# Optimization experiments

Measured on AMD Instinct MI355X. Metric: run time of the kernel, lower is better.

Reference implementation:

```python
import jax, jax.numpy as jnp
import numpy as np

EPS = 1e-5
NUM_GRAPHS = 64


def _linear(x, W, b):
    return x @ W + b


def setup_inputs() -> dict:
    key = jax.random.key(0)
    ks = jax.random.split(key, 32)
    N, E, IN, EF, H, ED, T, L, C = 25000, 400000, 128, 16, 32, 32, 4, 2, 1
    F = H            # F_in (divide_input=False)
    Fo = H // T      # F_out per tower

    def w(k, shape):
        return jax.random.normal(k, shape, jnp.float32) / np.sqrt(shape[-2])

    inp = {
        'x': jax.random.normal(ks[0], (N, IN), jnp.float32),
        'edge_attr': jax.random.normal(ks[1], (E, EF), jnp.float32),
        'edge_weight': jax.random.uniform(ks[2], (E,), jnp.float32),
        'edge_index': jax.random.randint(ks[3], (2, E), 0, N),
        'batch': jnp.sort(jax.random.randint(ks[4], (N,), 0, NUM_GRAPHS)),
        'node_W': w(ks[5], (IN, H)), 'node_b': jnp.zeros((H,), jnp.float32),
        'edge_W': w(ks[6], (EF, ED)), 'edge_b': jnp.zeros((ED,), jnp.float32),
        'enc_W': w(ks[7], (L, ED, F)), 'enc_b': jnp.zeros((L, F), jnp.float32),
        'pre_W': w(ks[8], (L, T, 3 * F, F)), 'pre_b': jnp.zeros((L, T, F), jnp.float32),
        'post_W': w(ks[9], (L, T, 13 * F, Fo)), 'post_b': jnp.zeros((L, T, Fo), jnp.float32),
        'lin_W': w(ks[10], (L, H, H)), 'lin_b': jnp.zeros((L, H), jnp.float32),
        'bn_g': jnp.ones((L, H), jnp.float32), 'bn_b': jnp.zeros((L, H), jnp.float32),
        'mlp_W1': w(ks[11], (H, H)), 'mlp_b1': jnp.zeros((H,), jnp.float32),
        'mlp_W2': w(ks[12], (H, H // 2)), 'mlp_b2': jnp.zeros((H // 2,), jnp.float32),
        'mlp_W3': w(ks[13], (H // 2, C)), 'mlp_b3': jnp.zeros((C,), jnp.float32),
    }
    return inp


def reference(x, edge_attr, edge_weight, node_W, node_b, edge_W, edge_b,
              enc_W, enc_b, pre_W, pre_b, post_W, post_b, lin_W, lin_b,
              bn_g, bn_b, mlp_W1, mlp_b1, mlp_W2, mlp_b2, mlp_W3, mlp_b3,
              edge_index, batch):
    N = x.shape[0]
    L, T = pre_W.shape[0], pre_W.shape[1]
    src, dst = edge_index[0], edge_index[1]

    # degree-based scalers (PNA): avg_deg_log = mean_n log(deg_n + 1)
    deg = jax.ops.segment_sum(jnp.ones((src.shape[0],), x.dtype), dst, num_segments=N)
    avg_deg_log = jnp.mean(jnp.log(deg + 1.0))
    degc = jnp.clip(deg, 1.0)[:, None, None]          # [N,1,1]
    log_deg = jnp.log(degc + 1.0)
    amp = log_deg / avg_deg_log                        # amplification scaler
    att = avg_deg_log / log_deg                        # attenuation scaler
    has_edge = (deg > 0)[:, None, None]

    h = _linear(x, node_W, node_b)                     # node_emb  [N,H]
    e = _linear(edge_attr, edge_W, edge_b)             # edge_emb  [E,ED]

    for l in range(L):
        el = _linear(e, enc_W[l], enc_b[l])            # edge_encoder [E,F]
        m_in = jnp.concatenate([h[dst], h[src], el], axis=-1)      # [E,3F]
        msg = jnp.einsum('ef,tfg->etg', m_in, pre_W[l]) + pre_b[l]  # per-tower pre_nn [E,T,F]
        msg = msg * edge_weight[:, None, None]
        s = jax.ops.segment_sum(msg, dst, num_segments=N)
        s2 = jax.ops.segment_sum(msg * msg, dst, num_segments=N)
        mean = s / degc
        std = jnp.sqrt(jax.nn.relu(s2 / degc - mean * mean) + EPS)
        mn = jnp.where(has_edge, jax.ops.segment_min(msg, dst, num_segments=N), 0.0)
        mx = jnp.where(has_edge, jax.ops.segment_max(msg, dst, num_segments=N), 0.0)
        agg = jnp.concatenate([mean, mn, mx, std], axis=-1)            # [N,T,4F]
        agg = jnp.concatenate([agg, agg * amp, agg * att], axis=-1)    # [N,T,12F]
        out = jnp.concatenate(
            [jnp.broadcast_to(h[:, None, :], (N, T, h.shape[-1])), agg], axis=-1)  # [N,T,13F]
        out = jnp.einsum('ntf,tfg->ntg', out, post_W[l]) + post_b[l]   # post_nn [N,T,Fo]
        out = out.reshape(N, -1) @ lin_W[l] + lin_b[l]                 # [N,H]
        mu = jnp.mean(out, axis=0)
        var = jnp.var(out, axis=0)
        out = (out - mu) / jnp.sqrt(var + EPS) * bn_g[l] + bn_b[l]     # BatchNorm (batch stats)
        h = jax.nn.relu(out)

    g = jax.ops.segment_sum(h, batch, num_segments=NUM_GRAPHS)        # global_add_pool
    g = jax.nn.relu(_linear(g, mlp_W1, mlp_b1))
    g = jax.nn.relu(_linear(g, mlp_W2, mlp_b2))
    return _linear(g, mlp_W3, mlp_b3)
```

## Files before the change

kernel.cpp:

```cpp
#include <hip/hip_runtime.h>

constexpr float kEps = 1e-5f;

__device__ __forceinline__ unsigned short f2bf(float x) {
  unsigned int u = __float_as_uint(x);
  unsigned int r = (u + 0x7fffu + ((u >> 16) & 1u)) >> 16;
  return (unsigned short)r;
}
__device__ __forceinline__ float bflo(unsigned int u) { return __uint_as_float(u << 16); }
__device__ __forceinline__ float bfhi(unsigned int u) { return __uint_as_float(u & 0xffff0000u); }
__device__ __forceinline__ unsigned int packbf(float a, float b) {
  return (unsigned int)f2bf(a) | ((unsigned int)f2bf(b) << 16);
}


__global__ void zero_int2(int* __restrict__ a, int* __restrict__ b, int n) {
  int i = blockIdx.x * blockDim.x + threadIdx.x;
  if (i < n) { a[i] = 0; b[i] = 0; }
}

__global__ void hist_kernel(const int* __restrict__ dst, int* __restrict__ deg, int E) {
  int e = blockIdx.x * blockDim.x + threadIdx.x;
  if (e < E) atomicAdd(&deg[dst[e]], 1);
}

__global__ void scan1_kernel(const int* __restrict__ deg, int* __restrict__ off,
                             int* __restrict__ part, int N) {
  __shared__ int sm[1024];
  int i = blockIdx.x * 1024 + threadIdx.x;
  int v = (i < N) ? deg[i] : 0;
  sm[threadIdx.x] = v;
  __syncthreads();
  for (int o = 1; o < 1024; o <<= 1) {
    int t = (threadIdx.x >= o) ? sm[threadIdx.x - o] : 0;
    __syncthreads();
    sm[threadIdx.x] += t;
    __syncthreads();
  }
  if (i < N) off[i] = sm[threadIdx.x] - v;
  if (threadIdx.x == 1023) part[blockIdx.x] = sm[1023];
}

__global__ void scan2_kernel(int* __restrict__ part, int* __restrict__ off, int nb, int N) {
  if (threadIdx.x == 0) {
    int run = 0;
    for (int b = 0; b < nb; b++) { int p = part[b]; part[b] = run; run += p; }
    off[N] = run;
  }
}

__global__ void scan3_kernel(int* __restrict__ off, const int* __restrict__ part, int N) {
  int i = blockIdx.x * 1024 + threadIdx.x;
  if (i < N) off[i] += part[blockIdx.x];
}

__global__ void fill_kernel(const int* __restrict__ src, const int* __restrict__ dst,
                            const float* __restrict__ ew, const int* __restrict__ off,
                            int* __restrict__ cnt, int* __restrict__ edg,
                            int* __restrict__ srcs, float* __restrict__ ews, int E) {
  int e = blockIdx.x * blockDim.x + threadIdx.x;
  if (e < E) {
    int d = dst[e];
    int slot = off[d] + atomicAdd(&cnt[d], 1);
    edg[slot] = e;
    srcs[slot] = src[e];
    ews[slot] = ew[e];
  }
}

__global__ void egather_kernel(const int* __restrict__ edg, const float4* __restrict__ eattr4,
                               float4* __restrict__ eattrg4, int E4) {
  int i = blockIdx.x * blockDim.x + threadIdx.x;
  if (i < E4) {
    int slot = i >> 2, quad = i & 3;
    int e = edg[slot];
    eattrg4[i] = eattr4[e * 4 + quad];
  }
}

__global__ void adl_kernel(const int* __restrict__ deg, float* __restrict__ adl, int N) {
  __shared__ float sm[1024];
  float s = 0.f;
  for (int n = threadIdx.x; n < N; n += 1024) s += logf((float)deg[n] + 1.f);
  sm[threadIdx.x] = s;
  __syncthreads();
  for (int o = 512; o > 0; o >>= 1) {
    if (threadIdx.x < o) sm[threadIdx.x] += sm[threadIdx.x + o];
    __syncthreads();
  }
  if (threadIdx.x == 0) adl[0] = sm[0];
}

__global__ void node_emb_kernel(const float* __restrict__ x, const float* __restrict__ W,
                                const float* __restrict__ b, float* __restrict__ h, int N) {
  int n = blockIdx.x * 8 + (threadIdx.x >> 5);
  int j = threadIdx.x & 31;
  if (n >= N) return;
  float acc = b[j];
  const float4* x4 = (const float4*)(x + (size_t)n * 128);
#pragma unroll
  for (int q = 0; q < 32; q++) {
    float4 v = x4[q];
    acc += v.x * W[(4 * q + 0) * 32 + j];
    acc += v.y * W[(4 * q + 1) * 32 + j];
    acc += v.z * W[(4 * q + 2) * 32 + j];
    acc += v.w * W[(4 * q + 3) * 32 + j];
  }
  h[n * 32 + j] = acc;
}

__global__ void fuse_kernel(const float* __restrict__ edge_W, const float* __restrict__ edge_b,
                            const float* __restrict__ enc_W, const float* __restrict__ enc_b,
                            const float* __restrict__ pre_W, const float* __restrict__ pre_b,
                            float* __restrict__ Wf, float* __restrict__ bf) {
  __shared__ float tW[2][16][32];
  __shared__ float tb[2][32];
  int tid = threadIdx.x;
  for (int i = tid; i < 1024; i += 256) {
    int l = i >> 9, r = (i >> 5) & 15, c = i & 31;
    float s = 0.f;
    for (int k = 0; k < 32; k++) s += edge_W[r * 32 + k] * enc_W[(l * 32 + k) * 32 + c];
    tW[l][r][c] = s;
  }
  for (int i = tid; i < 64; i += 256) {
    int l = i >> 5, c = i & 31;
    float s = enc_b[l * 32 + c];
    for (int k = 0; k < 32; k++) s += edge_b[k] * enc_W[(l * 32 + k) * 32 + c];
    tb[l][c] = s;
  }
  __syncthreads();
  for (int i = tid; i < 4096; i += 256) {
    int l = i >> 11, t = (i >> 9) & 3, r = (i >> 5) & 15, c = i & 31;
    float s = 0.f;
    for (int k = 0; k < 32; k++) s += tW[l][r][k] * pre_W[((l * 4 + t) * 96 + 64 + k) * 32 + c];
    Wf[i] = s;
  }
  for (int i = tid; i < 256; i += 256) {
    int l = i >> 7, t = (i >> 5) & 3, c = i & 31;
    float s = pre_b[(l * 4 + t) * 32 + c];
    for (int k = 0; k < 32; k++) s += tb[l][k] * pre_W[((l * 4 + t) * 96 + 64 + k) * 32 + c];
    bf[i] = s;
  }
}

__global__ __launch_bounds__(256) void prep_kernel(
    const float* __restrict__ h, const float* __restrict__ preW,
    const float* __restrict__ bfv, unsigned short* __restrict__ qB,
    unsigned short* __restrict__ AB, float* __restrict__ bn, int N) {
  if (blockIdx.x == 0 && threadIdx.x < 64) bn[threadIdx.x] = 0.f;
  __shared__ float hs[16][32];
  int tid = threadIdx.x;
  int c = tid & 127, half = tid >> 7;
  int t = c >> 5, g = c & 31;
  float ws[32], wd[32];
  {
    const float* pS = preW + (t * 96 + 32) * 32 + g;
    const float* pD = preW + (t * 96) * 32 + g;
#pragma unroll
    for (int k = 0; k < 32; k++) { ws[k] = pS[k * 32]; wd[k] = pD[k * 32]; }
  }
  float bc = bfv[c];
  int base = blockIdx.x * 16;
  for (int i = tid; i < 512; i += 256) {
    int nn = i >> 5;
    hs[nn][i & 31] = (base + nn < N) ? h[(size_t)(base + nn) * 32 + (i & 31)] : 0.f;
  }
  __syncthreads();
#pragma unroll
  for (int nn = 0; nn < 8; ++nn) {
    int nl = half + 2 * nn;
    int n = base + nl;
    if (n >= N) continue;
    float qa = 0.f, Aa = bc;
#pragma unroll
    for (int k = 0; k < 32; k++) {
      float hk = hs[nl][k];
      qa = fmaf(hk, ws[k], qa);
      Aa = fmaf(hk, wd[k], Aa);
    }
    qB[(size_t)n * 128 + c] = f2bf(qa);
    AB[(size_t)n * 128 + c] = f2bf(Aa);
  }
}

#define FOLD8(F0, F1, VA, VB, O)                                           \
  F0 = fmaf(VA.x, wfa[O + 0], F0); F1 = fmaf(VA.x, wfb[O + 0], F1);        \
  F0 = fmaf(VA.y, wfa[O + 1], F0); F1 = fmaf(VA.y, wfb[O + 1], F1);        \
  F0 = fmaf(VA.z, wfa[O + 2], F0); F1 = fmaf(VA.z, wfb[O + 2], F1);        \
  F0 = fmaf(VA.w, wfa[O + 3], F0); F1 = fmaf(VA.w, wfb[O + 3], F1);        \
  F0 = fmaf(VB.x, wfa[O + 4], F0); F1 = fmaf(VB.x, wfb[O + 4], F1);        \
  F0 = fmaf(VB.y, wfa[O + 5], F0); F1 = fmaf(VB.y, wfb[O + 5], F1);        \
  F0 = fmaf(VB.z, wfa[O + 6], F0); F1 = fmaf(VB.z, wfb[O + 6], F1);        \
  F0 = fmaf(VB.w, wfa[O + 7], F0); F1 = fmaf(VB.w, wfb[O + 7], F1);

#define STATACC(V0, V1)                                                    \
  s0a += V0; sq0 = fmaf(V0, V0, sq0); mn0 = fminf(mn0, V0); mx0 = fmaxf(mx0, V0); \
  s1a += V1; sq1 = fmaf(V1, V1, sq1); mn1 = fminf(mn1, V1); mx1 = fmaxf(mx1, V1);

__global__ __launch_bounds__(256, 4) void agg3_kernel(
    const unsigned int* __restrict__ qB, const unsigned int* __restrict__ AB,
    const int* __restrict__ coff, const int* __restrict__ srcs,
    const float* __restrict__ ews, const float* __restrict__ eattrg,
    const float* __restrict__ Wf, unsigned int* __restrict__ stats, int N) {
  int lane = threadIdx.x & 63;
  int n = (blockIdx.x * blockDim.x + threadIdx.x) >> 6;
  if (n >= N) return;
  int t = lane >> 4, g0 = (2 * lane) & 31;
  float wfa[16], wfb[16];
  {
    const float* p = Wf + t * 512 + g0;
#pragma unroll
    for (int k = 0; k < 16; k++) { wfa[k] = p[k * 32]; wfb[k] = p[k * 32 + 1]; }
  }
  unsigned int au = AB[(size_t)n * 64 + lane];
  float a0 = bflo(au), a1 = bfhi(au);
  int beg = coff[n], end = coff[n + 1];
  int dg = end - beg;
  float s0a = 0.f, s1a = 0.f, sq0 = 0.f, sq1 = 0.f;
  float mn0 = 1e30f, mn1 = 1e30f, mx0 = -1e30f, mx1 = -1e30f;

  int i = beg;
  int sc0 = 0, sc1 = 0, sc2 = 0, sc3 = 0;
  if (i + 4 <= end) { sc0 = srcs[i]; sc1 = srcs[i + 1]; sc2 = srcs[i + 2]; sc3 = srcs[i + 3]; }
  for (; i + 4 <= end; i += 4) {
    unsigned int q0 = qB[(size_t)sc0 * 64 + lane];
    unsigned int q1 = qB[(size_t)sc1 * 64 + lane];
    unsigned int q2 = qB[(size_t)sc2 * 64 + lane];
    unsigned int q3 = qB[(size_t)sc3 * 64 + lane];
    float w0 = ews[i], w1 = ews[i + 1], w2 = ews[i + 2], w3 = ews[i + 3];
    const float4* ep = (const float4*)(eattrg + (size_t)i * 16);
    if (i + 8 <= end) { sc0 = srcs[i + 4]; sc1 = srcs[i + 5]; sc2 = srcs[i + 6]; sc3 = srcs[i + 7]; }
    float f00 = 0.f, f10 = 0.f, f01 = 0.f, f11 = 0.f;
    float f02 = 0.f, f12 = 0.f, f03 = 0.f, f13 = 0.f;
    {
      float4 aA = ep[0], aB = ep[1], bA = ep[4], bB = ep[5];
      float4 cA = ep[8], cB = ep[9], dA = ep[12], dB = ep[13];
      FOLD8(f00, f10, aA, aB, 0)
      FOLD8(f01, f11, bA, bB, 0)
      FOLD8(f02, f12, cA, cB, 0)
      FOLD8(f03, f13, dA, dB, 0)
    }
    {
      float4 aA = ep[2], aB = ep[3], bA = ep[6], bB = ep[7];
      float4 cA = ep[10], cB = ep[11], dA = ep[14], dB = ep[15];
      FOLD8(f00, f10, aA, aB, 8)
      FOLD8(f01, f11, bA, bB, 8)
      FOLD8(f02, f12, cA, cB, 8)
      FOLD8(f03, f13, dA, dB, 8)
    }
    float v0, v1;
    v0 = (a0 + bflo(q0) + f00) * w0; v1 = (a1 + bfhi(q0) + f10) * w0; STATACC(v0, v1)
    v0 = (a0 + bflo(q1) + f01) * w1; v1 = (a1 + bfhi(q1) + f11) * w1; STATACC(v0, v1)
    v0 = (a0 + bflo(q2) + f02) * w2; v1 = (a1 + bfhi(q2) + f12) * w2; STATACC(v0, v1)
    v0 = (a0 + bflo(q3) + f03) * w3; v1 = (a1 + bfhi(q3) + f13) * w3; STATACC(v0, v1)
  }
  for (; i < end; ++i) {
    int s = srcs[i];
    unsigned int q = qB[(size_t)s * 64 + lane];
    float w = ews[i];
    const float4* ep = (const float4*)(eattrg + (size_t)i * 16);
    float4 aA = ep[0], aB = ep[1], cA = ep[2], cB = ep[3];
    float f0 = 0.f, f1 = 0.f;
    FOLD8(f0, f1, aA, aB, 0)
    FOLD8(f0, f1, cA, cB, 8)
    float v0 = (a0 + bflo(q) + f0) * w;
    float v1 = (a1 + bfhi(q) + f1) * w;
    STATACC(v0, v1)
  }
  if (dg == 0) { mn0 = 0.f; mx0 = 0.f; mn1 = 0.f; mx1 = 0.f; }
  float inv = 1.f / (float)(dg > 0 ? dg : 1);
  float mean0 = s0a * inv, mean1 = s1a * inv;
  float sd0 = sqrtf(fmaxf(sq0 * inv - mean0 * mean0, 0.f) + kEps);
  float sd1 = sqrtf(fmaxf(sq1 * inv - mean1 * mean1, 0.f) + kEps);
  unsigned int* sp = stats + (size_t)n * 256;
  sp[0 * 64 + lane] = packbf(mean0, mean1);
  sp[1 * 64 + lane] = packbf(mn0, mn1);
  sp[2 * 64 + lane] = packbf(mx0, mx1);
  sp[3 * 64 + lane] = packbf(sd0, sd1);
}

__global__ __launch_bounds__(256) void post_kernel(
    const float* __restrict__ h, const unsigned int* __restrict__ stats,
    const int* __restrict__ coff, const float* __restrict__ adl,
    const float* __restrict__ postW, const float* __restrict__ postB,
    const float* __restrict__ linW, const float* __restrict__ linB,
    float* __restrict__ pre, float* __restrict__ bn, int N) {
  __shared__ unsigned int pwp[208 * 32];
  __shared__ unsigned int stu[4][256];
  __shared__ float red[8][32];
  int tid = threadIdx.x;
  for (int i = tid; i < 6656; i += 256) {
    int r = i >> 5, cc = i & 31, tP = cc >> 3, gq = cc & 7;
    float lo = postW[tP * 3328 + (2 * r) * 8 + gq];
    float hi = postW[tP * 3328 + (2 * r + 1) * 8 + gq];
    pwp[i] = packbf(lo, hi);
  }
  __syncthreads();

  int wave = tid >> 6, lane = tid & 63;
  int c = lane & 31, hh = lane >> 5;
  int tP = c >> 3;
  float adN = adl[0];
  float bs = 0.f, bq = 0.f;

  for (int n = blockIdx.x * 4 + wave; n < N; n += gridDim.x * 4) {
    {
      uint4 su = ((const uint4*)stats)[(size_t)n * 64 + lane];
      ((uint4*)stu[wave])[lane] = su;
    }
    int dg = coff[n + 1] - coff[n];
    float degc = (float)(dg > 0 ? dg : 1);
    float ad = adN / (float)N;
    float ld = logf(degc + 1.f);
    float amp = ld / ad, att = ad / ld;

    float acc = (hh == 0) ? postB[tP * 8 + (c & 7)] : 0.f;
    const float4* h4 = (const float4*)(h + (size_t)n * 32);
#pragma unroll
    for (int q4 = 0; q4 < 4; q4++) {
      float4 hv = h4[hh * 4 + q4];
      int r0 = hh * 8 + q4 * 2;
      unsigned int u0 = pwp[r0 * 32 + c], u1 = pwp[(r0 + 1) * 32 + c];
      acc = fmaf(hv.x, bflo(u0), acc);
      acc = fmaf(hv.y, bfhi(u0), acc);
      acc = fmaf(hv.z, bflo(u1), acc);
      acc = fmaf(hv.w, bfhi(u1), acc);
    }
#pragma unroll 8
    for (int jj = 0; jj < 32; jj++) {
      int sIdx = hh * 2 + (jj >> 4);
      unsigned int sv = stu[wave][sIdx * 64 + tP * 16 + (jj & 15)];
      float v0 = bflo(sv), v1 = bfhi(sv);
      int rm = 16 + hh * 32 + jj, ra = 80 + hh * 32 + jj, rt = 144 + hh * 32 + jj;
      unsigned int um = pwp[rm * 32 + c];
      unsigned int ua = pwp[ra * 32 + c];
      unsigned int ut = pwp[rt * 32 + c];
      float w0 = bflo(um); w0 = fmaf(amp, bflo(ua), w0); w0 = fmaf(att, bflo(ut), w0);
      float w1 = bfhi(um); w1 = fmaf(amp, bfhi(ua), w1); w1 = fmaf(att, bfhi(ut), w1);
      acc = fmaf(v0, w0, acc);
      acc = fmaf(v1, w1, acc);
    }
    acc += __shfl_xor(acc, 32);
    float o = linB[c];
#pragma unroll
    for (int k = 0; k < 32; k++) {
      float a = __shfl(acc, k);
      o = fmaf(a, linW[k * 32 + c], o);
    }
    if (lane < 32) {
      pre[(size_t)n * 32 + c] = o;
      bs += o;
      bq = fmaf(o, o, bq);
    }
  }

  __syncthreads();
  if (lane < 32) {
    red[wave * 2 + 0][c] = bs;
    red[wave * 2 + 1][c] = bq;
  }
  __syncthreads();
  if (tid < 64) {
    int which = tid >> 5, cc = tid & 31;
    float s = red[0 * 2 + which][cc] + red[1 * 2 + which][cc] +
              red[2 * 2 + which][cc] + red[3 * 2 + which][cc];
    atomicAdd(&bn[which * 32 + cc], s);
  }
}

__global__ void bn_apply_kernel(const float* __restrict__ pre, const float* __restrict__ bn,
                                const float* __restrict__ gamma, const float* __restrict__ beta,
                                float* __restrict__ h, int N) {
  int i = blockIdx.x * 256 + threadIdx.x;
  if (i >= N * 32) return;
  int j = i & 31;
  float invN = 1.f / (float)N;
  float mu = bn[j] * invN;
  float var = bn[32 + j] * invN - mu * mu;
  float is = rsqrtf(var + kEps);
  float v = (pre[i] - mu) * is * gamma[j] + beta[j];
  h[i] = fmaxf(v, 0.f);
}


__device__ __forceinline__ int lower_bound_dev(const int* a, int n, int key) {
  int lo = 0, hi = n;
  while (lo < hi) {
    int m = (lo + hi) >> 1;
    if (a[m] < key) lo = m + 1; else hi = m;
  }
  return lo;
}

__global__ void pool_kernel(const float* __restrict__ h, const int* __restrict__ batch,
                            float* __restrict__ gp, int N) {
  int gi = blockIdx.x;
  int lo = lower_bound_dev(batch, N, gi);
  int hi = lower_bound_dev(batch, N, gi + 1);
  __shared__ float part[8][32];
  int j = threadIdx.x & 31, ch = threadIdx.x >> 5;
  float s = 0.f;
  for (int n = lo + ch; n < hi; n += 8) s += h[(size_t)n * 32 + j];
  part[ch][j] = s;
  __syncthreads();
  if (threadIdx.x < 32) {
    float t = 0.f;
    for (int c2 = 0; c2 < 8; c2++) t += part[c2][j];
    gp[gi * 32 + j] = t;
  }
}

__global__ void mlp_kernel(const float* __restrict__ gp,
                           const float* __restrict__ W1, const float* __restrict__ b1,
                           const float* __restrict__ W2, const float* __restrict__ b2,
                           const float* __restrict__ W3, const float* __restrict__ b3,
                           float* __restrict__ out) {
  __shared__ float g1[64 * 32];
  __shared__ float g2[64 * 16];
  int tid = threadIdx.x;
  for (int i = tid; i < 2048; i += 256) {
    int r = i >> 5, c = i & 31;
    float s = b1[c];
    for (int k = 0; k < 32; k++) s += gp[r * 32 + k] * W1[k * 32 + c];
    g1[i] = fmaxf(s, 0.f);
  }
  __syncthreads();
  for (int i = tid; i < 1024; i += 256) {
    int r = i >> 4, c = i & 15;
    float s = b2[c];
    for (int k = 0; k < 32; k++) s += g1[r * 32 + k] * W2[k * 16 + c];
    g2[i] = fmaxf(s, 0.f);
  }
  __syncthreads();
  if (tid < 64) {
    float s = b3[0];
    for (int k = 0; k < 16; k++) s += g2[tid * 16 + k] * W3[k];
    out[tid] = s;
  }
}


extern "C" void kernel_launch(void* const* d_in, const int* in_sizes, int n_in,
                              void* d_out, int out_size, void* d_ws, size_t ws_size,
                              hipStream_t stream) {
  (void)n_in; (void)out_size; (void)ws_size;
  const float* x     = (const float*)d_in[0];
  const float* eattr = (const float*)d_in[1];
  const float* ew    = (const float*)d_in[2];
  const int*   eidx  = (const int*)d_in[3];
  const int*   batch = (const int*)d_in[4];
  const float* nodeW = (const float*)d_in[5];
  const float* nodeB = (const float*)d_in[6];
  const float* edgeW = (const float*)d_in[7];
  const float* edgeB = (const float*)d_in[8];
  const float* encW  = (const float*)d_in[9];
  const float* encB  = (const float*)d_in[10];
  const float* preW  = (const float*)d_in[11];
  const float* preB  = (const float*)d_in[12];
  const float* postW = (const float*)d_in[13];
  const float* postB = (const float*)d_in[14];
  const float* linW  = (const float*)d_in[15];
  const float* linB  = (const float*)d_in[16];
  const float* bnG   = (const float*)d_in[17];
  const float* bnB   = (const float*)d_in[18];
  const float* W1    = (const float*)d_in[19];
  const float* b1    = (const float*)d_in[20];
  const float* W2    = (const float*)d_in[21];
  const float* b2    = (const float*)d_in[22];
  const float* W3    = (const float*)d_in[23];
  const float* b3    = (const float*)d_in[24];
  float* out = (float*)d_out;

  int N = in_sizes[0] / 128;
  int E = in_sizes[2];
  const int* srcp = eidx;
  const int* dstp = eidx + E;

  char* wsb = (char*)d_ws;
  size_t woff = 0;
  auto alloc = [&](size_t bytes) -> void* {
    void* p = (void*)(wsb + woff);
    woff += (bytes + 255) & ~(size_t)255;
    return p;
  };
  int* deg   = (int*)alloc((size_t)N * 4);
  int* cnt   = (int*)alloc((size_t)N * 4);
  int* coff  = (int*)alloc((size_t)(N + 1) * 4);
  int* part  = (int*)alloc(64 * 4);
  int* edg   = (int*)alloc((size_t)E * 4);
  int* srcs  = (int*)alloc((size_t)E * 4);
  float* ews = (float*)alloc((size_t)E * 4);
  float* eattrg = (float*)alloc((size_t)E * 16 * 4);
  float* h    = (float*)alloc((size_t)N * 32 * 4);
  float* pre  = (float*)alloc((size_t)N * 32 * 4);
  float* adl  = (float*)alloc(256);
  float* bn   = (float*)alloc(64 * 4);
  float* gp   = (float*)alloc(64 * 32 * 4);
  float* WfB  = (float*)alloc(2 * 4 * 16 * 32 * 4);
  float* bfB  = (float*)alloc(2 * 4 * 32 * 4);
  unsigned short* qB  = (unsigned short*)alloc((size_t)N * 128 * 2);
  unsigned short* AB  = (unsigned short*)alloc((size_t)N * 128 * 2);
  unsigned int* stats = (unsigned int*)alloc((size_t)N * 256 * 4);

  int nb = (N + 1023) / 1024;
  zero_int2<<<(N + 255) / 256, 256, 0, stream>>>(deg, cnt, N);
  hist_kernel<<<(E + 255) / 256, 256, 0, stream>>>(dstp, deg, E);
  scan1_kernel<<<nb, 1024, 0, stream>>>(deg, coff, part, N);
  scan2_kernel<<<1, 64, 0, stream>>>(part, coff, nb, N);
  scan3_kernel<<<nb, 1024, 0, stream>>>(coff, part, N);
  fill_kernel<<<(E + 255) / 256, 256, 0, stream>>>(srcp, dstp, ew, coff, cnt, edg, srcs, ews, E);
  egather_kernel<<<(E * 4 + 255) / 256, 256, 0, stream>>>(edg, (const float4*)eattr,
                                                          (float4*)eattrg, E * 4);
  adl_kernel<<<1, 1024, 0, stream>>>(deg, adl, N);
  node_emb_kernel<<<(N + 7) / 8, 256, 0, stream>>>(x, nodeW, nodeB, h, N);
  fuse_kernel<<<1, 256, 0, stream>>>(edgeW, edgeB, encW, encB, preW, preB, WfB, bfB);

  for (int l = 0; l < 2; l++) {
    prep_kernel<<<(N + 15) / 16, 256, 0, stream>>>(
        h, preW + (size_t)l * 12288, bfB + (size_t)l * 128, qB, AB, bn, N);
    agg3_kernel<<<(N + 3) / 4, 256, 0, stream>>>(
        (const unsigned int*)qB, (const unsigned int*)AB, coff, srcs, ews,
        eattrg, WfB + (size_t)l * 2048, stats, N);
    post_kernel<<<1280, 256, 0, stream>>>(
        h, stats, coff, adl,
        postW + (size_t)l * 13312, postB + (size_t)l * 32,
        linW + (size_t)l * 1024, linB + (size_t)l * 32, pre, bn, N);
    bn_apply_kernel<<<(N * 32 + 255) / 256, 256, 0, stream>>>(pre, bn, bnG + (size_t)l * 32,
                                                              bnB + (size_t)l * 32, h, N);
  }
  pool_kernel<<<64, 256, 0, stream>>>(h, batch, gp, N);
  mlp_kernel<<<1, 256, 0, stream>>>(gp, W1, b1, W2, b2, W3, b3, out);
}
```

Baseline: 453.4 us.

## Fuse edge-attr gather into fill, fuse BN apply with next prep, pack agg math

The edge-attribute gather now happens inside the CSR fill kernel, which removes the edg index array and one launch. The layer-0 batch-norm apply is fused into the layer-1 prep kernel, and the BN stat buffers are zeroed up front instead of inside prep. The aggregation kernel uses packed 2-wide float vector FMA/min/max, prefetches edge weights alongside sources, adds a sched barrier, and drops the occupancy hint from 4 to 3 blocks. The trade-off is fewer launches and less global memory traffic, at the cost of scattered 64-byte writes in fill and possibly lower agg occupancy.

```diff
diff --git a/kernel.cpp b/kernel.cpp
--- a/kernel.cpp
+++ b/kernel.cpp
@@ -1,6 +1,8 @@
 #include <hip/hip_runtime.h>
 
 constexpr float kEps = 1e-5f;
+
+typedef float f2v __attribute__((ext_vector_type(2)));
 
 __device__ __forceinline__ unsigned short f2bf(float x) {
   unsigned int u = __float_as_uint(x);
@@ -12,11 +14,18 @@
 __device__ __forceinline__ unsigned int packbf(float a, float b) {
   return (unsigned int)f2bf(a) | ((unsigned int)f2bf(b) << 16);
 }
-
-
-__global__ void zero_int2(int* __restrict__ a, int* __restrict__ b, int n) {
+__device__ __forceinline__ f2v fma2(f2v a, f2v b, f2v c) { return __builtin_elementwise_fma(a, b, c); }
+__device__ __forceinline__ f2v splat2(float x) { f2v r; r.x = x; r.y = x; return r; }
+__device__ __forceinline__ f2v unpk(unsigned int u) { f2v r; r.x = bflo(u); r.y = bfhi(u); return r; }
+__device__ __forceinline__ f2v min2(f2v a, f2v b) { return __builtin_elementwise_min(a, b); }
+__device__ __forceinline__ f2v max2(f2v a, f2v b) { return __builtin_elementwise_max(a, b); }
+
+
+__global__ void zero_kernel(int* __restrict__ a, int* __restrict__ b,
+                            float* __restrict__ bnb, int n) {
   int i = blockIdx.x * blockDim.x + threadIdx.x;
   if (i < n) { a[i] = 0; b[i] = 0; }
+  if (i < 128) bnb[i] = 0.f;
 }
 
 __global__ void hist_kernel(const int* __restrict__ dst, int* __restrict__ deg, int E) {
@@ -55,26 +64,22 @@
 }
 
 __global__ void fill_kernel(const int* __restrict__ src, const int* __restrict__ dst,
-                            const float* __restrict__ ew, const int* __restrict__ off,
-                            int* __restrict__ cnt, int* __restrict__ edg,
-                            int* __restrict__ srcs, float* __restrict__ ews, int E) {
+                            const float* __restrict__ ew, const float4* __restrict__ eattr4,
+                            const int* __restrict__ off, int* __restrict__ cnt,
+                            int* __restrict__ srcs, float* __restrict__ ews,
+                            float4* __restrict__ eattrg4, int E) {
   int e = blockIdx.x * blockDim.x + threadIdx.x;
   if (e < E) {
     int d = dst[e];
     int slot = off[d] + atomicAdd(&cnt[d], 1);
-    edg[slot] = e;
     srcs[slot] = src[e];
     ews[slot] = ew[e];
-  }
-}
-
-__global__ void egather_kernel(const int* __restrict__ edg, const float4* __restrict__ eattr4,
-                               float4* __restrict__ eattrg4, int E4) {
-  int i = blockIdx.x * blockDim.x + threadIdx.x;
-  if (i < E4) {
-    int slot = i >> 2, quad = i & 3;
-    int e = edg[slot];
-    eattrg4[i] = eattr4[e * 4 + quad];
+    float4 a = eattr4[e * 4 + 0], b = eattr4[e * 4 + 1];
+    float4 c = eattr4[e * 4 + 2], q = eattr4[e * 4 + 3];
+    eattrg4[(size_t)slot * 4 + 0] = a;
+    eattrg4[(size_t)slot * 4 + 1] = b;
+    eattrg4[(size_t)slot * 4 + 2] = c;
+    eattrg4[(size_t)slot * 4 + 3] = q;
   }
 }
 
@@ -146,8 +151,7 @@
 __global__ __launch_bounds__(256) void prep_kernel(
     const float* __restrict__ h, const float* __restrict__ preW,
     const float* __restrict__ bfv, unsigned short* __restrict__ qB,
-    unsigned short* __restrict__ AB, float* __restrict__ bn, int N) {
-  if (blockIdx.x == 0 && threadIdx.x < 64) bn[threadIdx.x] = 0.f;
+    unsigned short* __restrict__ AB, int N) {
   __shared__ float hs[16][32];
   int tid = threadIdx.x;
   int c = tid & 127, half = tid >> 7;
@@ -183,21 +187,71 @@
   }
 }
 
-#define FOLD8(F0, F1, VA, VB, O)                                           \
-  F0 = fmaf(VA.x, wfa[O + 0], F0); F1 = fmaf(VA.x, wfb[O + 0], F1);        \
-  F0 = fmaf(VA.y, wfa[O + 1], F0); F1 = fmaf(VA.y, wfb[O + 1], F1);        \
-  F0 = fmaf(VA.z, wfa[O + 2], F0); F1 = fmaf(VA.z, wfb[O + 2], F1);        \
-  F0 = fmaf(VA.w, wfa[O + 3], F0); F1 = fmaf(VA.w, wfb[O + 3], F1);        \
-  F0 = fmaf(VB.x, wfa[O + 4], F0); F1 = fmaf(VB.x, wfb[O + 4], F1);        \
-  F0 = fmaf(VB.y, wfa[O + 5], F0); F1 = fmaf(VB.y, wfb[O + 5], F1);        \
-  F0 = fmaf(VB.z, wfa[O + 6], F0); F1 = fmaf(VB.z, wfb[O + 6], F1);        \
-  F0 = fmaf(VB.w, wfa[O + 7], F0); F1 = fmaf(VB.w, wfb[O + 7], F1);
-
-#define STATACC(V0, V1)                                                    \
-  s0a += V0; sq0 = fmaf(V0, V0, sq0); mn0 = fminf(mn0, V0); mx0 = fmaxf(mx0, V0); \
-  s1a += V1; sq1 = fmaf(V1, V1, sq1); mn1 = fminf(mn1, V1); mx1 = fmaxf(mx1, V1);
-
-__global__ __launch_bounds__(256, 4) void agg3_kernel(
+__global__ __launch_bounds__(256) void bnprep_kernel(
+    const float* __restrict__ pre, const float* __restrict__ bnv,
+    const float* __restrict__ gamma, const float* __restrict__ beta,
+    const float* __restrict__ preW, const float* __restrict__ bfv,
+    float* __restrict__ h, unsigned short* __restrict__ qB,
+    unsigned short* __restrict__ AB, int N) {
+  __shared__ float hs[16][32];
+  int tid = threadIdx.x;
+  int base = blockIdx.x * 16;
+  float invN = 1.f / (float)N;
+  for (int idx = tid; idx < 512; idx += 256) {
+    int nn = idx >> 5, j = idx & 31;
+    int n = base + nn;
+    float v = 0.f;
+    if (n < N) {
+      float mu = bnv[j] * invN;
+      float var = bnv[32 + j] * invN - mu * mu;
+      float is = rsqrtf(var + kEps);
+      v = fmaxf((pre[(size_t)n * 32 + j] - mu) * is * gamma[j] + beta[j], 0.f);
+      h[(size_t)n * 32 + j] = v;
+    }
+    hs[nn][j] = v;
+  }
+  int c = tid & 127, half = tid >> 7;
+  int t = c >> 5, g = c & 31;
+  float ws[32], wd[32];
+  {
+    const float* pS = preW + (t * 96 + 32) * 32 + g;
+    const float* pD = preW + (t * 96) * 32 + g;
+#pragma unroll
+    for (int k = 0; k < 32; k++) { ws[k] = pS[k * 32]; wd[k] = pD[k * 32]; }
+  }
+  float bc = bfv[c];
+  __syncthreads();
+#pragma unroll
+  for (int nn = 0; nn < 8; ++nn) {
+    int nl = half + 2 * nn;
+    int n = base + nl;
+    if (n >= N) continue;
+    float qa = 0.f, Aa = bc;
+#pragma unroll
+    for (int k = 0; k < 32; k++) {
+      float hk = hs[nl][k];
+      qa = fmaf(hk, ws[k], qa);
+      Aa = fmaf(hk, wd[k], Aa);
+    }
+    qB[(size_t)n * 128 + c] = f2bf(qa);
+    AB[(size_t)n * 128 + c] = f2bf(Aa);
+  }
+}
+
+#define FOLDE(F, EA, EB, EC, ED)                                \
+  F = fma2(splat2(EA.x), wf[0], F);  F = fma2(splat2(EA.y), wf[1], F);  \
+  F = fma2(splat2(EA.z), wf[2], F);  F = fma2(splat2(EA.w), wf[3], F);  \
+  F = fma2(splat2(EB.x), wf[4], F);  F = fma2(splat2(EB.y), wf[5], F);  \
+  F = fma2(splat2(EB.z), wf[6], F);  F = fma2(splat2(EB.w), wf[7], F);  \
+  F = fma2(splat2(EC.x), wf[8], F);  F = fma2(splat2(EC.y), wf[9], F);  \
+  F = fma2(splat2(EC.z), wf[10], F); F = fma2(splat2(EC.w), wf[11], F); \
+  F = fma2(splat2(ED.x), wf[12], F); F = fma2(splat2(ED.y), wf[13], F); \
+  F = fma2(splat2(ED.z), wf[14], F); F = fma2(splat2(ED.w), wf[15], F);
+
+#define STAT2(V)                                                \
+  sum = sum + V; sq = fma2(V, V, sq); mn = min2(mn, V); mx = max2(mx, V);
+
+__global__ __launch_bounds__(256, 3) void agg4_kernel(
     const unsigned int* __restrict__ qB, const unsigned int* __restrict__ AB,
     const int* __restrict__ coff, const int* __restrict__ srcs,
     const float* __restrict__ ews, const float* __restrict__ eattrg,
@@ -206,76 +260,73 @@
   int n = (blockIdx.x * blockDim.x + threadIdx.x) >> 6;
   if (n >= N) return;
   int t = lane >> 4, g0 = (2 * lane) & 31;
-  float wfa[16], wfb[16];
+  f2v wf[16];
   {
     const float* p = Wf + t * 512 + g0;
 #pragma unroll
-    for (int k = 0; k < 16; k++) { wfa[k] = p[k * 32]; wfb[k] = p[k * 32 + 1]; }
-  }
-  unsigned int au = AB[(size_t)n * 64 + lane];
-  float a0 = bflo(au), a1 = bfhi(au);
+    for (int k = 0; k < 16; k++) { f2v r; r.x = p[k * 32]; r.y = p[k * 32 + 1]; wf[k] = r; }
+  }
+  f2v a = unpk(AB[(size_t)n * 64 + lane]);
   int beg = coff[n], end = coff[n + 1];
   int dg = end - beg;
-  float s0a = 0.f, s1a = 0.f, sq0 = 0.f, sq1 = 0.f;
-  float mn0 = 1e30f, mn1 = 1e30f, mx0 = -1e30f, mx1 = -1e30f;
+  f2v sum = splat2(0.f), sq = splat2(0.f);
+  f2v mn = splat2(1e30f), mx = splat2(-1e30f);
 
   int i = beg;
   int sc0 = 0, sc1 = 0, sc2 = 0, sc3 = 0;
-  if (i + 4 <= end) { sc0 = srcs[i]; sc1 = srcs[i + 1]; sc2 = srcs[i + 2]; sc3 = srcs[i + 3]; }
+  float w0 = 0.f, w1 = 0.f, w2 = 0.f, w3 = 0.f;
+  if (i + 4 <= end) {
+    sc0 = srcs[i]; sc1 = srcs[i + 1]; sc2 = srcs[i + 2]; sc3 = srcs[i + 3];
+    w0 = ews[i]; w1 = ews[i + 1]; w2 = ews[i + 2]; w3 = ews[i + 3];
+  }
   for (; i + 4 <= end; i += 4) {
     unsigned int q0 = qB[(size_t)sc0 * 64 + lane];
     unsigned int q1 = qB[(size_t)sc1 * 64 + lane];
     unsigned int q2 = qB[(size_t)sc2 * 64 + lane];
     unsigned int q3 = qB[(size_t)sc3 * 64 + lane];
-    float w0 = ews[i], w1 = ews[i + 1], w2 = ews[i + 2], w3 = ews[i + 3];
     const float4* ep = (const float4*)(eattrg + (size_t)i * 16);
-    if (i + 8 <= end) { sc0 = srcs[i + 4]; sc1 = srcs[i + 5]; sc2 = srcs[i + 6]; sc3 = srcs[i + 7]; }
-    float f00 = 0.f, f10 = 0.f, f01 = 0.f, f11 = 0.f;
-    float f02 = 0.f, f12 = 0.f, f03 = 0.f, f13 = 0.f;
-    {
-      float4 aA = ep[0], aB = ep[1], bA = ep[4], bB = ep[5];
-      float4 cA = ep[8], cB = ep[9], dA = ep[12], dB = ep[13];
-      FOLD8(f00, f10, aA, aB, 0)
-      FOLD8(f01, f11, bA, bB, 0)
-      FOLD8(f02, f12, cA, cB, 0)
-      FOLD8(f03, f13, dA, dB, 0)
-    }
-    {
-      float4 aA = ep[2], aB = ep[3], bA = ep[6], bB = ep[7];
-      float4 cA = ep[10], cB = ep[11], dA = ep[14], dB = ep[15];
-      FOLD8(f00, f10, aA, aB, 8)
-      FOLD8(f01, f11, bA, bB, 8)
-      FOLD8(f02, f12, cA, cB, 8)
-      FOLD8(f03, f13, dA, dB, 8)
-    }
-    float v0, v1;
-    v0 = (a0 + bflo(q0) + f00) * w0; v1 = (a1 + bfhi(q0) + f10) * w0; STATACC(v0, v1)
-    v0 = (a0 + bflo(q1) + f01) * w1; v1 = (a1 + bfhi(q1) + f11) * w1; STATACC(v0, v1)
-    v0 = (a0 + bflo(q2) + f02) * w2; v1 = (a1 + bfhi(q2) + f12) * w2; STATACC(v0, v1)
-    v0 = (a0 + bflo(q3) + f03) * w3; v1 = (a1 + bfhi(q3) + f13) * w3; STATACC(v0, v1)
+    float4 e0 = ep[0], e1 = ep[1], e2 = ep[2], e3 = ep[3];
+    float4 e4 = ep[4], e5 = ep[5], e6 = ep[6], e7 = ep[7];
+    float4 e8 = ep[8], e9 = ep[9], e10 = ep[10], e11 = ep[11];
+    float4 e12 = ep[12], e13 = ep[13], e14 = ep[14], e15 = ep[15];
+    float wc0 = w0, wc1 = w1, wc2 = w2, wc3 = w3;
+    if (i + 8 <= end) {
+      sc0 = srcs[i + 4]; sc1 = srcs[i + 5]; sc2 = srcs[i + 6]; sc3 = srcs[i + 7];
+      w0 = ews[i + 4]; w1 = ews[i + 5]; w2 = ews[i + 6]; w3 = ews[i + 7];
+    }
+    __builtin_amdgcn_sched_barrier(0);
+    f2v f0 = splat2(0.f), f1 = splat2(0.f), f2_ = splat2(0.f), f3 = splat2(0.f);
+    FOLDE(f0, e0, e1, e2, e3)
+    FOLDE(f1, e4, e5, e6, e7)
+    FOLDE(f2_, e8, e9, e10, e11)
+    FOLDE(f3, e12, e13, e14, e15)
+    f2v v;
+    v = (a + unpk(q0) + f0) * splat2(wc0); STAT2(v)
+    v = (a + unpk(q1) + f1) * splat2(wc1); STAT2(v)
+    v = (a + unpk(q2) + f2_) * splat2(wc2); STAT2(v)
+    v = (a + unpk(q3) + f3) * splat2(wc3); STAT2(v)
   }
   for (; i < end; ++i) {
     int s = srcs[i];
+    float w = ews[i];
     unsigned int q = qB[(size_t)s * 64 + lane];
-    float w = ews[i];
     const float4* ep = (const float4*)(eattrg + (size_t)i * 16);
-    float4 aA = ep[0], aB = ep[1], cA = ep[2], cB = ep[3];
-    float f0 = 0.f, f1 = 0.f;
-    FOLD8(f0, f1, aA, aB, 0)
-    FOLD8(f0, f1, cA, cB, 8)
-    float v0 = (a0 + bflo(q) + f0) * w;
-    float v1 = (a1 + bfhi(q) + f1) * w;
-    STATACC(v0, v1)
-  }
-  if (dg == 0) { mn0 = 0.f; mx0 = 0.f; mn1 = 0.f; mx1 = 0.f; }
+    float4 ea = ep[0], eb = ep[1], ec = ep[2], ed = ep[3];
+    f2v f = splat2(0.f);
+    FOLDE(f, ea, eb, ec, ed)
+    f2v v = (a + unpk(q) + f) * splat2(w);
+    STAT2(v)
+  }
+  if (dg == 0) { mn = splat2(0.f); mx = splat2(0.f); }
   float inv = 1.f / (float)(dg > 0 ? dg : 1);
-  float mean0 = s0a * inv, mean1 = s1a * inv;
-  float sd0 = sqrtf(fmaxf(sq0 * inv - mean0 * mean0, 0.f) + kEps);
-  float sd1 = sqrtf(fmaxf(sq1 * inv - mean1 * mean1, 0.f) + kEps);
+  f2v mean = sum * splat2(inv);
+  f2v var = sq * splat2(inv) - mean * mean;
+  float sd0 = sqrtf(fmaxf(var.x, 0.f) + kEps);
+  float sd1 = sqrtf(fmaxf(var.y, 0.f) + kEps);
   unsigned int* sp = stats + (size_t)n * 256;
-  sp[0 * 64 + lane] = packbf(mean0, mean1);
-  sp[1 * 64 + lane] = packbf(mn0, mn1);
-  sp[2 * 64 + lane] = packbf(mx0, mx1);
+  sp[0 * 64 + lane] = packbf(mean.x, mean.y);
+  sp[1 * 64 + lane] = packbf(mn.x, mn.y);
+  sp[2 * 64 + lane] = packbf(mx.x, mx.y);
   sp[3 * 64 + lane] = packbf(sd0, sd1);
 }
 
@@ -487,14 +538,13 @@
   int* cnt   = (int*)alloc((size_t)N * 4);
   int* coff  = (int*)alloc((size_t)(N + 1) * 4);
   int* part  = (int*)alloc(64 * 4);
-  int* edg   = (int*)alloc((size_t)E * 4);
   int* srcs  = (int*)alloc((size_t)E * 4);
   float* ews = (float*)alloc((size_t)E * 4);
   float* eattrg = (float*)alloc((size_t)E * 16 * 4);
   float* h    = (float*)alloc((size_t)N * 32 * 4);
   float* pre  = (float*)alloc((size_t)N * 32 * 4);
   float* adl  = (float*)alloc(256);
-  float* bn   = (float*)alloc(64 * 4);
+  float* bnbuf = (float*)alloc(2 * 64 * 4);
   float* gp   = (float*)alloc(64 * 32 * 4);
   float* WfB  = (float*)alloc(2 * 4 * 16 * 32 * 4);
   float* bfB  = (float*)alloc(2 * 4 * 32 * 4);
@@ -503,31 +553,34 @@
   unsigned int* stats = (unsigned int*)alloc((size_t)N * 256 * 4);
 
   int nb = (N + 1023) / 1024;
-  zero_int2<<<(N + 255) / 256, 256, 0, stream>>>(deg, cnt, N);
+  zero_kernel<<<(N + 255) / 256, 256, 0, stream>>>(deg, cnt, bnbuf, N);
   hist_kernel<<<(E + 255) / 256, 256, 0, stream>>>(dstp, deg, E);
   scan1_kernel<<<nb, 1024, 0, stream>>>(deg, coff, part, N);
   scan2_kernel<<<1, 64, 0, stream>>>(part, coff, nb, N);
   scan3_kernel<<<nb, 1024, 0, stream>>>(coff, part, N);
-  fill_kernel<<<(E + 255) / 256, 256, 0, stream>>>(srcp, dstp, ew, coff, cnt, edg, srcs, ews, E);
-  egather_kernel<<<(E * 4 + 255) / 256, 256, 0, stream>>>(edg, (const float4*)eattr,
-                                                          (float4*)eattrg, E * 4);
+  fill_kernel<<<(E + 255) / 256, 256, 0, stream>>>(srcp, dstp, ew, (const float4*)eattr,
+                                                   coff, cnt, srcs, ews, (float4*)eattrg, E);
   adl_kernel<<<1, 1024, 0, stream>>>(deg, adl, N);
   node_emb_kernel<<<(N + 7) / 8, 256, 0, stream>>>(x, nodeW, nodeB, h, N);
   fuse_kernel<<<1, 256, 0, stream>>>(edgeW, edgeB, encW, encB, preW, preB, WfB, bfB);
 
-  for (int l = 0; l < 2; l++) {
-    prep_kernel<<<(N + 15) / 16, 256, 0, stream>>>(
-        h, preW + (size_t)l * 12288, bfB + (size_t)l * 128, qB, AB, bn, N);
-    agg3_kernel<<<(N + 3) / 4, 256, 0, stream>>>(
-        (const unsigned int*)qB, (const unsigned int*)AB, coff, srcs, ews,
-        eattrg, WfB + (size_t)l * 2048, stats, N);
-    post_kernel<<<1280, 256, 0, stream>>>(
-        h, stats, coff, adl,
-        postW + (size_t)l * 13312, postB + (size_t)l * 32,
-        linW + (size_t)l * 1024, linB + (size_t)l * 32, pre, bn, N);
-    bn_apply_kernel<<<(N * 32 + 255) / 256, 256, 0, stream>>>(pre, bn, bnG + (size_t)l * 32,
-                                                              bnB + (size_t)l * 32, h, N);
-  }
+  prep_kernel<<<(N + 15) / 16, 256, 0, stream>>>(h, preW, bfB, qB, AB, N);
+  agg4_kernel<<<(N + 3) / 4, 256, 0, stream>>>(
+      (const unsigned int*)qB, (const unsigned int*)AB, coff, srcs, ews,
+      eattrg, WfB, stats, N);
+  post_kernel<<<1280, 256, 0, stream>>>(
+      h, stats, coff, adl, postW, postB, linW, linB, pre, bnbuf, N);
+  bnprep_kernel<<<(N + 15) / 16, 256, 0, stream>>>(
+      pre, bnbuf, bnG, bnB, preW + 12288, bfB + 128, h, qB, AB, N);
+  agg4_kernel<<<(N + 3) / 4, 256, 0, stream>>>(
+      (const unsigned int*)qB, (const unsigned int*)AB, coff, srcs, ews,
+      eattrg, WfB + 2048, stats, N);
+  post_kernel<<<1280, 256, 0, stream>>>(
+      h, stats, coff, adl, postW + 13312, postB + 32, linW + 1024, linB + 32,
+      pre, bnbuf + 64, N);
+  bn_apply_kernel<<<(N * 32 + 255) / 256, 256, 0, stream>>>(
+      pre, bnbuf + 64, bnG + 32, bnB + 32, h, N);
+
   pool_kernel<<<64, 256, 0, stream>>>(h, batch, gp, N);
   mlp_kernel<<<1, 256, 0, stream>>>(gp, W1, b1, W2, b2, W3, b3, out);
 }
```

New measurement: 454.2 us. Within noise of the previous version (+0.2%).
